# Performance work log

Hardware: AMD Instinct MI355X
Metric: run time of the kernel (lower is better)

The kernel has to match this reference:

```python
import jax, jax.numpy as jnp
import numpy as np

EPS = 1e-5

def ter_quant(w):
    # BitNet b1.58 absmean ternary quantization: scale by mean(|W|), round to {-1,0,1}, rescale.
    gamma = jnp.mean(jnp.abs(w)) + EPS
    wq = jnp.clip(jnp.round(w / gamma), -1.0, 1.0) * gamma
    return wq

def setup_inputs() -> dict:
    key = jax.random.key(0)
    k_x, k_w1, k_w2 = jax.random.split(key, 3)
    B, S, D, H = 64, 197, 768, 3072
    x = jax.random.normal(k_x, (B, S, D), dtype=jnp.float32)
    w1 = jax.random.normal(k_w1, (H, D), dtype=jnp.float32) * (1.0 / np.sqrt(D))
    b1 = jnp.zeros((H,), dtype=jnp.float32)
    w2 = jax.random.normal(k_w2, (D, H), dtype=jnp.float32) * (1.0 / np.sqrt(H))
    b2 = jnp.zeros((D,), dtype=jnp.float32)
    return {"x": x, "w1": w1, "b1": b1, "w2": w2, "b2": b2}

def reference(x, w1, b1, w2, b2):
    # fc1: ternary-quantized linear, exact GELU, fc2: ternary-quantized linear (dropout p=0 is identity)
    h = jnp.einsum('bsd,hd->bsh', x, ter_quant(w1)) + b1
    h = jax.nn.gelu(h, approximate=False)
    y = jnp.einsum('bsh,dh->bsd', h, ter_quant(w2)) + b2
    return y
```

## Files before the change

kernel.cpp:

```cpp
#include <hip/hip_runtime.h>
#include <hip/hip_bf16.h>
#include <math.h>

typedef __bf16 bf16_t;
typedef __bf16 bf16x8 __attribute__((ext_vector_type(8)));
typedef __bf16 bf16x4 __attribute__((ext_vector_type(4)));
typedef float f32x4 __attribute__((ext_vector_type(4)));

#define QEPS 1e-5

__device__ __forceinline__ void gload_lds16(const void* g, void* l) {
  __builtin_amdgcn_global_load_lds((const __attribute__((address_space(1))) void*)g,
                                   (__attribute__((address_space(3))) void*)l, 16, 0, 0);
}

__device__ __forceinline__ float gelu_exact(float x) {
  float a = x * 0.7071067811865476f;
  float s = fabsf(a);
  float t = __builtin_amdgcn_rcpf(__builtin_fmaf(0.3275911f, s, 1.0f));
  float p = __builtin_fmaf(1.061405429f, t, -1.453152027f);
  p = __builtin_fmaf(p, t, 1.421413741f);
  p = __builtin_fmaf(p, t, -0.284496736f);
  p = __builtin_fmaf(p, t, 0.254829592f);
  p = p * t;
  float e = __expf(-s * s);
  float er = copysignf(__builtin_fmaf(-p, e, 1.0f), a);
  return 0.5f * x * (1.0f + er);
}

__global__ void reduce_part_kernel(const float* __restrict__ w1, const float* __restrict__ w2,
                                   int n, double* __restrict__ part) {
  const bool second = blockIdx.x >= 256;
  const float* __restrict__ w = second ? w2 : w1;
  const int b = second ? blockIdx.x - 256 : blockIdx.x;
  double s = 0.0;
  const int stride = 256 * 256 * 4;
  for (int i = (b * 256 + threadIdx.x) * 4; i < n; i += stride) {
    float4 v = *(const float4*)(w + i);
    s += (double)fabsf(v.x) + (double)fabsf(v.y) + (double)fabsf(v.z) + (double)fabsf(v.w);
  }
  for (int off = 32; off > 0; off >>= 1)
    s += __shfl_down(s, off, 64);
  __shared__ double ls[4];
  int lane = threadIdx.x & 63, wv = threadIdx.x >> 6;
  if (lane == 0) ls[wv] = s;
  __syncthreads();
  if (threadIdx.x == 0) part[blockIdx.x] = ls[0] + ls[1] + ls[2] + ls[3];
}

__global__ void prep_kernel(const float* __restrict__ w1, const float* __restrict__ w2,
                            const float* __restrict__ x, const double* __restrict__ part,
                            int nW, long long nxv, bf16_t* __restrict__ q1,
                            bf16_t* __restrict__ q2, bf16_t* __restrict__ xb,
                            double* __restrict__ gammas) {
  const int QB = (nW >> 1) >> 8;
  const int tid = threadIdx.x;
  if (blockIdx.x < QB) {
    const int half = QB >> 1;
    const bool second = blockIdx.x >= half;
    double p = part[(second ? 256 : 0) + tid];
    for (int off = 32; off > 0; off >>= 1)
      p += __shfl_down(p, off, 64);
    __shared__ double red[4];
    if ((tid & 63) == 0) red[tid >> 6] = p;
    __syncthreads();
    const double g = (red[0] + red[1] + red[2] + red[3]) / (double)nW + QEPS;
    if (tid == 0 && blockIdx.x == (second ? half : 0)) gammas[second ? 1 : 0] = g;
    const double rg = 1.0 / g;
    const int idx = blockIdx.x * 256 + tid - (second ? (nW >> 2) : 0);
    const float4 v = ((const float4*)(second ? w2 : w1))[idx];
    bf16x4 r;
    r[0] = (bf16_t)(float)fmin(1.0, fmax(-1.0, rint((double)v.x * rg)));
    r[1] = (bf16_t)(float)fmin(1.0, fmax(-1.0, rint((double)v.y * rg)));
    r[2] = (bf16_t)(float)fmin(1.0, fmax(-1.0, rint((double)v.z * rg)));
    r[3] = (bf16_t)(float)fmin(1.0, fmax(-1.0, rint((double)v.w * rg)));
    ((bf16x4*)(second ? q2 : q1))[idx] = r;
  } else {
    long long i = ((long long)(blockIdx.x - QB) * 256 + tid) * 4;
    bf16x4 r;
    if (i < nxv) {
      float4 v = *(const float4*)(x + i);
      r[0] = (bf16_t)v.x; r[1] = (bf16_t)v.y; r[2] = (bf16_t)v.z; r[3] = (bf16_t)v.w;
    } else {
      r[0] = (bf16_t)0.0f; r[1] = (bf16_t)0.0f; r[2] = (bf16_t)0.0f; r[3] = (bf16_t)0.0f;
    }
    *(bf16x4*)(xb + i) = r;
  }
}

template <int EPI, int BN>
__global__ __launch_bounds__(256, 4)
void gemm_bt_kernel(const bf16_t* __restrict__ A, const bf16_t* __restrict__ B,
                    const float* __restrict__ bias, const double* __restrict__ gptr,
                    void* __restrict__ Cout, int N, int K, int Mvalid, int gx) {
  constexpr int NJ = BN / 32;
  __shared__ bf16_t sA[128 * 64];
  __shared__ bf16_t sB[BN * 64];

  const int G = gridDim.x;
  const int f = blockIdx.x;
  const int xcd = f & 7;
  const int idx = f >> 3;
  const int q8 = G >> 3, r8 = G & 7;
  const int t = xcd * q8 + (xcd < r8 ? xcd : r8) + idx;
  const int bx = t % gx;
  const int by = t / gx;

  const int tid = threadIdx.x;
  const int lane = tid & 63;
  const int wave = tid >> 6;
  const int wr = (wave >> 1) * 64;
  const int wc = (wave & 1) * (BN / 2);
  const int row16 = lane & 15;
  const int quad = lane >> 4;

  const size_t Ks = (size_t)K;
  const int cg = (tid & 7) ^ ((tid >> 3) & 7);
  const bf16_t* gA = A + ((size_t)(by * 128 + (tid >> 3))) * Ks + (size_t)cg * 8;
  const bf16_t* gB = B + ((size_t)(bx * BN + (tid >> 3))) * Ks + (size_t)cg * 8;
  bf16_t* lA = sA + wave * 512;
  bf16_t* lB = sB + wave * 512;

  f32x4 acc[4][NJ] = {};

  for (int k0 = 0; k0 < K; k0 += 64) {
#pragma unroll
    for (int n = 0; n < 4; n++)
      gload_lds16(gA + (size_t)(n * 32) * Ks, lA + n * 2048);
#pragma unroll
    for (int n = 0; n < BN / 32; n++)
      gload_lds16(gB + (size_t)(n * 32) * Ks, lB + n * 2048);
    gA += 64;
    gB += 64;
    __syncthreads();

#pragma unroll
    for (int kk = 0; kk < 2; kk++) {
      bf16x8 afr[4], bfr[NJ];
      const int swz = ((kk * 4 + quad) ^ (row16 & 7)) * 8;
#pragma unroll
      for (int i = 0; i < 4; i++)
        afr[i] = *(const bf16x8*)&sA[(wr + i * 16 + row16) * 64 + swz];
#pragma unroll
      for (int j = 0; j < NJ; j++)
        bfr[j] = *(const bf16x8*)&sB[(wc + j * 16 + row16) * 64 + swz];
#pragma unroll
      for (int i = 0; i < 4; i++)
#pragma unroll
        for (int j = 0; j < NJ; j++)
          acc[i][j] = __builtin_amdgcn_mfma_f32_16x16x32_bf16(afr[i], bfr[j], acc[i][j], 0, 0, 0);
    }
    __syncthreads();
  }

  const float gamma = (float)gptr[0];
  const int c_base = bx * BN + wc + row16;
  const int r_base = by * 128 + wr + quad * 4;

  if constexpr (EPI == 0) {
    bf16_t* sE = sA;
    float bv[NJ];
#pragma unroll
    for (int j = 0; j < NJ; j++) bv[j] = bias[c_base + j * 16];
    bf16_t* h = (bf16_t*)Cout;
#pragma unroll
    for (int i = 0; i < 4; i++) {
#pragma unroll
      for (int j = 0; j < NJ; j++) {
        const int col = wc + j * 16 + row16;
#pragma unroll
        for (int r = 0; r < 4; r++) {
          const int e = (wave >> 1) * 16 + quad * 4 + r;
          float v = gelu_exact(gamma * acc[i][j][r] + bv[j]);
          sE[e * 136 + col] = (bf16_t)v;
        }
      }
      __syncthreads();
      {
        const int e = tid >> 3, ch = tid & 7;
        const int grow = by * 128 + (e >> 4) * 64 + i * 16 + (e & 15);
        bf16_t* dst = &h[(size_t)grow * N + bx * BN];
        *(bf16x8*)&dst[ch * 8] = *(const bf16x8*)&sE[e * 136 + ch * 8];
        *(bf16x8*)&dst[ch * 8 + 64] = *(const bf16x8*)&sE[e * 136 + ch * 8 + 64];
      }
      __syncthreads();
    }
  } else {
    float* out = (float*)Cout;
#pragma unroll
    for (int j = 0; j < NJ; j++) {
      const int col = c_base + j * 16;
      const float bv = bias[col];
#pragma unroll
      for (int i = 0; i < 4; i++) {
#pragma unroll
        for (int r = 0; r < 4; r++) {
          const int row = r_base + i * 16 + r;
          if (row < Mvalid)
            out[(size_t)row * N + col] = gamma * acc[i][j][r] + bv;
        }
      }
    }
  }
}

extern "C" void kernel_launch(void* const* d_in, const int* in_sizes, int n_in,
                              void* d_out, int out_size, void* d_ws, size_t ws_size,
                              hipStream_t stream) {
  const float* x  = (const float*)d_in[0];
  const float* w1 = (const float*)d_in[1];
  const float* b1 = (const float*)d_in[2];
  const float* w2 = (const float*)d_in[3];
  const float* b2 = (const float*)d_in[4];
  float* out = (float*)d_out;

  const int M = 64 * 197;
  const int Mpad = 12672;
  const int D = 768, H = 3072;
  const int nW = H * D;

  char* ws = (char*)d_ws;
  double* part = (double*)ws;
  double* gammas = (double*)(ws + 4096);
  bf16_t* xb  = (bf16_t*)(ws + 4096 + 256);
  bf16_t* w1q = xb + (size_t)Mpad * D;
  bf16_t* w2q = w1q + (size_t)H * D;
  bf16_t* hb  = w2q + (size_t)D * H;

  reduce_part_kernel<<<512, 256, 0, stream>>>(w1, w2, nW, part);
  const int QB = (nW >> 1) >> 8;
  const int CB = (int)(((long long)Mpad * D / 4) / 256);
  prep_kernel<<<QB + CB, 256, 0, stream>>>(w1, w2, x, part, nW, (long long)M * D,
                                           w1q, w2q, xb, gammas);

  const int gy = Mpad / 128;
  const int gx1 = H / 128;
  const int gx2 = D / 64;
  gemm_bt_kernel<0, 128><<<gx1 * gy, 256, 0, stream>>>(xb, w1q, b1, gammas + 0, hb, H, D, M, gx1);
  gemm_bt_kernel<1, 64><<<gx2 * gy, 256, 0, stream>>>(hb, w2q, b2, gammas + 1, out, D, H, M, gx2);
}
```

Before: 258.4 us.

## Double-buffer LDS tiles in GEMM and use 128x128 tiles for both GEMMs

Adds two LDS stages so the global-to-LDS loads for the next K slice are issued before computing on the current slice, which overlaps memory latency with MFMA work and removes one barrier per iteration. The second GEMM moves from 128x64 to 128x128 tiles, giving more reuse of each loaded tile. LDS use grows to 64KB per block and launch bounds drop to 2 blocks per CU, which reduces occupancy. The fc2 grid also becomes smaller (6 column tiles), which may leave the machine less evenly loaded.

```diff
diff --git a/kernel.cpp b/kernel.cpp
--- a/kernel.cpp
+++ b/kernel.cpp
@@ -88,14 +88,12 @@
   }
 }
 
-template <int EPI, int BN>
-__global__ __launch_bounds__(256, 4)
+template <int EPI>
+__global__ __launch_bounds__(256, 2)
 void gemm_bt_kernel(const bf16_t* __restrict__ A, const bf16_t* __restrict__ B,
                     const float* __restrict__ bias, const double* __restrict__ gptr,
                     void* __restrict__ Cout, int N, int K, int Mvalid, int gx) {
-  constexpr int NJ = BN / 32;
-  __shared__ bf16_t sA[128 * 64];
-  __shared__ bf16_t sB[BN * 64];
+  __shared__ bf16_t sm[2][2][128 * 64];
 
   const int G = gridDim.x;
   const int f = blockIdx.x;
@@ -110,63 +108,75 @@
   const int lane = tid & 63;
   const int wave = tid >> 6;
   const int wr = (wave >> 1) * 64;
-  const int wc = (wave & 1) * (BN / 2);
+  const int wc = (wave & 1) * 64;
   const int row16 = lane & 15;
   const int quad = lane >> 4;
 
   const size_t Ks = (size_t)K;
   const int cg = (tid & 7) ^ ((tid >> 3) & 7);
   const bf16_t* gA = A + ((size_t)(by * 128 + (tid >> 3))) * Ks + (size_t)cg * 8;
-  const bf16_t* gB = B + ((size_t)(bx * BN + (tid >> 3))) * Ks + (size_t)cg * 8;
-  bf16_t* lA = sA + wave * 512;
-  bf16_t* lB = sB + wave * 512;
-
-  f32x4 acc[4][NJ] = {};
-
+  const bf16_t* gB = B + ((size_t)(bx * 128 + (tid >> 3))) * Ks + (size_t)cg * 8;
+  const int lofs = wave * 512;
+
+  f32x4 acc[4][4] = {};
+
+#pragma unroll
+  for (int n = 0; n < 4; n++) {
+    gload_lds16(gA + (size_t)(n * 32) * Ks, &sm[0][0][lofs + n * 2048]);
+    gload_lds16(gB + (size_t)(n * 32) * Ks, &sm[0][1][lofs + n * 2048]);
+  }
+  gA += 64;
+  gB += 64;
+  __syncthreads();
+
+  int p = 0;
   for (int k0 = 0; k0 < K; k0 += 64) {
-#pragma unroll
-    for (int n = 0; n < 4; n++)
-      gload_lds16(gA + (size_t)(n * 32) * Ks, lA + n * 2048);
-#pragma unroll
-    for (int n = 0; n < BN / 32; n++)
-      gload_lds16(gB + (size_t)(n * 32) * Ks, lB + n * 2048);
-    gA += 64;
-    gB += 64;
-    __syncthreads();
-
+    if (k0 + 64 < K) {
+#pragma unroll
+      for (int n = 0; n < 4; n++) {
+        gload_lds16(gA + (size_t)(n * 32) * Ks, &sm[p ^ 1][0][lofs + n * 2048]);
+        gload_lds16(gB + (size_t)(n * 32) * Ks, &sm[p ^ 1][1][lofs + n * 2048]);
+      }
+      gA += 64;
+      gB += 64;
+    }
+
+    const bf16_t* sA = sm[p][0];
+    const bf16_t* sB = sm[p][1];
 #pragma unroll
     for (int kk = 0; kk < 2; kk++) {
-      bf16x8 afr[4], bfr[NJ];
+      bf16x8 afr[4], bfr[4];
       const int swz = ((kk * 4 + quad) ^ (row16 & 7)) * 8;
 #pragma unroll
       for (int i = 0; i < 4; i++)
         afr[i] = *(const bf16x8*)&sA[(wr + i * 16 + row16) * 64 + swz];
 #pragma unroll
-      for (int j = 0; j < NJ; j++)
+      for (int j = 0; j < 4; j++)
         bfr[j] = *(const bf16x8*)&sB[(wc + j * 16 + row16) * 64 + swz];
 #pragma unroll
       for (int i = 0; i < 4; i++)
 #pragma unroll
-        for (int j = 0; j < NJ; j++)
+        for (int j = 0; j < 4; j++)
           acc[i][j] = __builtin_amdgcn_mfma_f32_16x16x32_bf16(afr[i], bfr[j], acc[i][j], 0, 0, 0);
     }
     __syncthreads();
+    p ^= 1;
   }
 
   const float gamma = (float)gptr[0];
-  const int c_base = bx * BN + wc + row16;
+  const int c_base = bx * 128 + wc + row16;
   const int r_base = by * 128 + wr + quad * 4;
 
   if constexpr (EPI == 0) {
-    bf16_t* sE = sA;
-    float bv[NJ];
-#pragma unroll
-    for (int j = 0; j < NJ; j++) bv[j] = bias[c_base + j * 16];
+    bf16_t* sE = &sm[0][0][0];
+    float bv[4];
+#pragma unroll
+    for (int j = 0; j < 4; j++) bv[j] = bias[c_base + j * 16];
     bf16_t* h = (bf16_t*)Cout;
 #pragma unroll
     for (int i = 0; i < 4; i++) {
 #pragma unroll
-      for (int j = 0; j < NJ; j++) {
+      for (int j = 0; j < 4; j++) {
         const int col = wc + j * 16 + row16;
 #pragma unroll
         for (int r = 0; r < 4; r++) {
@@ -179,7 +189,7 @@
       {
         const int e = tid >> 3, ch = tid & 7;
         const int grow = by * 128 + (e >> 4) * 64 + i * 16 + (e & 15);
-        bf16_t* dst = &h[(size_t)grow * N + bx * BN];
+        bf16_t* dst = &h[(size_t)grow * N + bx * 128];
         *(bf16x8*)&dst[ch * 8] = *(const bf16x8*)&sE[e * 136 + ch * 8];
         *(bf16x8*)&dst[ch * 8 + 64] = *(const bf16x8*)&sE[e * 136 + ch * 8 + 64];
       }
@@ -188,7 +198,7 @@
   } else {
     float* out = (float*)Cout;
 #pragma unroll
-    for (int j = 0; j < NJ; j++) {
+    for (int j = 0; j < 4; j++) {
       const int col = c_base + j * 16;
       const float bv = bias[col];
 #pragma unroll
@@ -235,7 +245,7 @@
 
   const int gy = Mpad / 128;
   const int gx1 = H / 128;
-  const int gx2 = D / 64;
-  gemm_bt_kernel<0, 128><<<gx1 * gy, 256, 0, stream>>>(xb, w1q, b1, gammas + 0, hb, H, D, M, gx1);
-  gemm_bt_kernel<1, 64><<<gx2 * gy, 256, 0, stream>>>(hb, w2q, b2, gammas + 1, out, D, H, M, gx2);
-}
+  const int gx2 = D / 128;
+  gemm_bt_kernel<0><<<gx1 * gy, 256, 0, stream>>>(xb, w1q, b1, gammas + 0, hb, H, D, M, gx1);
+  gemm_bt_kernel<1><<<gx2 * gy, 256, 0, stream>>>(hb, w2q, b2, gammas + 1, out, D, H, M, gx2);
+}
```

New measurement: 279.6 us. 8.2% more time.

## Pre-tile operands into swizzled K-chunks and double-buffer LDS in GEMMs

Applied to the files above, without the earlier changes.

The prep kernel now writes x, w1q and w2q into a blocked layout of 128x32 tiles with an XOR swizzle. GEMM1's epilogue writes h in the same blocked layout, so each GEMM loads contiguous 8KB tiles and LDS is double-buffered over K=32 steps, with one barrier per step. GEMM1 tile width grows to 256 columns, giving fewer blocks with more accumulators each. This is meant to overlap global loads with MFMA work and get fully coalesced loads, at the cost of more LDS per block, lower occupancy and hardcoded problem sizes.

```diff
diff --git a/kernel.cpp b/kernel.cpp
--- a/kernel.cpp
+++ b/kernel.cpp
@@ -4,7 +4,6 @@
 
 typedef __bf16 bf16_t;
 typedef __bf16 bf16x8 __attribute__((ext_vector_type(8)));
-typedef __bf16 bf16x4 __attribute__((ext_vector_type(4)));
 typedef float f32x4 __attribute__((ext_vector_type(4)));
 
 #define QEPS 1e-5
@@ -50,52 +49,70 @@
 
 __global__ void prep_kernel(const float* __restrict__ w1, const float* __restrict__ w2,
                             const float* __restrict__ x, const double* __restrict__ part,
-                            int nW, long long nxv, bf16_t* __restrict__ q1,
-                            bf16_t* __restrict__ q2, bf16_t* __restrict__ xb,
-                            double* __restrict__ gammas) {
-  const int QB = (nW >> 1) >> 8;
+                            double* __restrict__ gammas, bf16_t* __restrict__ q1,
+                            bf16_t* __restrict__ q2, bf16_t* __restrict__ xb) {
   const int tid = threadIdx.x;
-  if (blockIdx.x < QB) {
-    const int half = QB >> 1;
-    const bool second = blockIdx.x >= half;
+  const int b = blockIdx.x;
+  if (b < 2304) {
+    const bool second = b >= 1152;
     double p = part[(second ? 256 : 0) + tid];
     for (int off = 32; off > 0; off >>= 1)
       p += __shfl_down(p, off, 64);
     __shared__ double red[4];
     if ((tid & 63) == 0) red[tid >> 6] = p;
     __syncthreads();
-    const double g = (red[0] + red[1] + red[2] + red[3]) / (double)nW + QEPS;
-    if (tid == 0 && blockIdx.x == (second ? half : 0)) gammas[second ? 1 : 0] = g;
+    const double g = (red[0] + red[1] + red[2] + red[3]) / 2359296.0 + QEPS;
+    if (tid == 0 && (b == 0 || b == 1152)) gammas[second ? 1 : 0] = g;
     const double rg = 1.0 / g;
-    const int idx = blockIdx.x * 256 + tid - (second ? (nW >> 2) : 0);
-    const float4 v = ((const float4*)(second ? w2 : w1))[idx];
-    bf16x4 r;
-    r[0] = (bf16_t)(float)fmin(1.0, fmax(-1.0, rint((double)v.x * rg)));
-    r[1] = (bf16_t)(float)fmin(1.0, fmax(-1.0, rint((double)v.y * rg)));
-    r[2] = (bf16_t)(float)fmin(1.0, fmax(-1.0, rint((double)v.z * rg)));
-    r[3] = (bf16_t)(float)fmin(1.0, fmax(-1.0, rint((double)v.w * rg)));
-    ((bf16x4*)(second ? q2 : q1))[idx] = r;
+    const int gchunk = (second ? b - 1152 : b) * 256 + tid;
+    const int tile = gchunk >> 9, cidx = gchunk & 511;
+    const int r = cidx >> 2, slot = cidx & 3, cch = slot ^ (r & 3);
+    int row, colbase, C;
+    if (second) { C = 3072; row = (tile / 96) * 128 + r; colbase = (tile % 96) * 32 + cch * 8; }
+    else        { C = 768;  row = (tile / 24) * 128 + r; colbase = (tile % 24) * 32 + cch * 8; }
+    const float* __restrict__ W = second ? w2 : w1;
+    const float4 v0 = *(const float4*)(W + (size_t)row * C + colbase);
+    const float4 v1 = *(const float4*)(W + (size_t)row * C + colbase + 4);
+    bf16x8 o;
+    o[0] = (bf16_t)(float)fmin(1.0, fmax(-1.0, rint((double)v0.x * rg)));
+    o[1] = (bf16_t)(float)fmin(1.0, fmax(-1.0, rint((double)v0.y * rg)));
+    o[2] = (bf16_t)(float)fmin(1.0, fmax(-1.0, rint((double)v0.z * rg)));
+    o[3] = (bf16_t)(float)fmin(1.0, fmax(-1.0, rint((double)v0.w * rg)));
+    o[4] = (bf16_t)(float)fmin(1.0, fmax(-1.0, rint((double)v1.x * rg)));
+    o[5] = (bf16_t)(float)fmin(1.0, fmax(-1.0, rint((double)v1.y * rg)));
+    o[6] = (bf16_t)(float)fmin(1.0, fmax(-1.0, rint((double)v1.z * rg)));
+    o[7] = (bf16_t)(float)fmin(1.0, fmax(-1.0, rint((double)v1.w * rg)));
+    *(bf16x8*)((second ? q2 : q1) + (size_t)gchunk * 8) = o;
   } else {
-    long long i = ((long long)(blockIdx.x - QB) * 256 + tid) * 4;
-    bf16x4 r;
-    if (i < nxv) {
-      float4 v = *(const float4*)(x + i);
-      r[0] = (bf16_t)v.x; r[1] = (bf16_t)v.y; r[2] = (bf16_t)v.z; r[3] = (bf16_t)v.w;
+    const int gchunk = (b - 2304) * 256 + tid;
+    const int tile = gchunk >> 9, cidx = gchunk & 511;
+    const int r = cidx >> 2, slot = cidx & 3, cch = slot ^ (r & 3);
+    const int row = (tile / 24) * 128 + r;
+    const int colbase = (tile % 24) * 32 + cch * 8;
+    bf16x8 o;
+    if (row < 12608) {
+      const float4 v0 = *(const float4*)(x + (size_t)row * 768 + colbase);
+      const float4 v1 = *(const float4*)(x + (size_t)row * 768 + colbase + 4);
+      o[0] = (bf16_t)v0.x; o[1] = (bf16_t)v0.y; o[2] = (bf16_t)v0.z; o[3] = (bf16_t)v0.w;
+      o[4] = (bf16_t)v1.x; o[5] = (bf16_t)v1.y; o[6] = (bf16_t)v1.z; o[7] = (bf16_t)v1.w;
     } else {
-      r[0] = (bf16_t)0.0f; r[1] = (bf16_t)0.0f; r[2] = (bf16_t)0.0f; r[3] = (bf16_t)0.0f;
-    }
-    *(bf16x4*)(xb + i) = r;
-  }
-}
-
-template <int EPI, int BN>
-__global__ __launch_bounds__(256, 4)
-void gemm_bt_kernel(const bf16_t* __restrict__ A, const bf16_t* __restrict__ B,
-                    const float* __restrict__ bias, const double* __restrict__ gptr,
-                    void* __restrict__ Cout, int N, int K, int Mvalid, int gx) {
-  constexpr int NJ = BN / 32;
-  __shared__ bf16_t sA[128 * 64];
-  __shared__ bf16_t sB[BN * 64];
+      o = bf16x8{};
+    }
+    *(bf16x8*)(xb + (size_t)gchunk * 8) = o;
+  }
+}
+
+template <int EPI, int NJ>
+__global__ __launch_bounds__(256, (NJ == 8 ? 2 : 3))
+void gemm_tiled(const bf16_t* __restrict__ A, const bf16_t* __restrict__ B,
+                const float* __restrict__ bias, const double* __restrict__ gptr,
+                void* __restrict__ Cout, int nkt, int gx, int Mvalid, int aux) {
+  constexpr int BN = NJ * 32;
+  constexpr int BTILE = BN * 32;
+  constexpr int NRTB = BN / 128;
+  __shared__ bf16_t sm[2 * 4096 + 2 * BTILE];
+  bf16_t* const sA0 = sm;
+  bf16_t* const sB0 = sm + 2 * 4096;
 
   const int G = gridDim.x;
   const int f = blockIdx.x;
@@ -114,55 +131,72 @@
   const int row16 = lane & 15;
   const int quad = lane >> 4;
 
-  const size_t Ks = (size_t)K;
-  const int cg = (tid & 7) ^ ((tid >> 3) & 7);
-  const bf16_t* gA = A + ((size_t)(by * 128 + (tid >> 3))) * Ks + (size_t)cg * 8;
-  const bf16_t* gB = B + ((size_t)(bx * BN + (tid >> 3))) * Ks + (size_t)cg * 8;
-  bf16_t* lA = sA + wave * 512;
-  bf16_t* lB = sB + wave * 512;
+  const bf16_t* gA = A + ((size_t)by * nkt) * 4096 + tid * 8;
+  const bf16_t* gB0 = B + ((size_t)(bx * NRTB) * nkt) * 4096 + tid * 8;
+  const bf16_t* gB1 = (NJ == 8) ? B + ((size_t)(bx * NRTB + 1) * nkt) * 4096 + tid * 8 : nullptr;
+  const int lws = wave * 512;
 
   f32x4 acc[4][NJ] = {};
 
-  for (int k0 = 0; k0 < K; k0 += 64) {
-#pragma unroll
-    for (int n = 0; n < 4; n++)
-      gload_lds16(gA + (size_t)(n * 32) * Ks, lA + n * 2048);
-#pragma unroll
-    for (int n = 0; n < BN / 32; n++)
-      gload_lds16(gB + (size_t)(n * 32) * Ks, lB + n * 2048);
-    gA += 64;
-    gB += 64;
+  {
+    gload_lds16(gA, sA0 + lws);
+    gload_lds16(gA + 2048, sA0 + 2048 + lws);
+    gload_lds16(gB0, sB0 + lws);
+    gload_lds16(gB0 + 2048, sB0 + 2048 + lws);
+    if constexpr (NJ == 8) {
+      gload_lds16(gB1, sB0 + 4096 + lws);
+      gload_lds16(gB1 + 2048, sB0 + 6144 + lws);
+    }
+    gA += 4096; gB0 += 4096;
+    if constexpr (NJ == 8) gB1 += 4096;
+  }
+  __syncthreads();
+
+  int p = 0;
+  const int sw = (quad ^ (row16 & 3)) * 8;
+  for (int kt = 0; kt < nkt; kt++) {
+    if (kt + 1 < nkt) {
+      bf16_t* dA = sA0 + (p ^ 1) * 4096;
+      bf16_t* dB = sB0 + (p ^ 1) * BTILE;
+      gload_lds16(gA, dA + lws);
+      gload_lds16(gA + 2048, dA + 2048 + lws);
+      gload_lds16(gB0, dB + lws);
+      gload_lds16(gB0 + 2048, dB + 2048 + lws);
+      if constexpr (NJ == 8) {
+        gload_lds16(gB1, dB + 4096 + lws);
+        gload_lds16(gB1 + 2048, dB + 6144 + lws);
+      }
+      gA += 4096; gB0 += 4096;
+      if constexpr (NJ == 8) gB1 += 4096;
+    }
+    const bf16_t* sA = sA0 + p * 4096;
+    const bf16_t* sB = sB0 + p * BTILE;
+    bf16x8 afr[4], bfr[NJ];
+#pragma unroll
+    for (int i = 0; i < 4; i++)
+      afr[i] = *(const bf16x8*)&sA[(wr + i * 16 + row16) * 32 + sw];
+#pragma unroll
+    for (int j = 0; j < NJ; j++)
+      bfr[j] = *(const bf16x8*)&sB[(wc + j * 16 + row16) * 32 + sw];
+#pragma unroll
+    for (int i = 0; i < 4; i++)
+#pragma unroll
+      for (int j = 0; j < NJ; j++)
+        acc[i][j] = __builtin_amdgcn_mfma_f32_16x16x32_bf16(afr[i], bfr[j], acc[i][j], 0, 0, 0);
     __syncthreads();
-
-#pragma unroll
-    for (int kk = 0; kk < 2; kk++) {
-      bf16x8 afr[4], bfr[NJ];
-      const int swz = ((kk * 4 + quad) ^ (row16 & 7)) * 8;
-#pragma unroll
-      for (int i = 0; i < 4; i++)
-        afr[i] = *(const bf16x8*)&sA[(wr + i * 16 + row16) * 64 + swz];
-#pragma unroll
-      for (int j = 0; j < NJ; j++)
-        bfr[j] = *(const bf16x8*)&sB[(wc + j * 16 + row16) * 64 + swz];
-#pragma unroll
-      for (int i = 0; i < 4; i++)
-#pragma unroll
-        for (int j = 0; j < NJ; j++)
-          acc[i][j] = __builtin_amdgcn_mfma_f32_16x16x32_bf16(afr[i], bfr[j], acc[i][j], 0, 0, 0);
-    }
-    __syncthreads();
+    p ^= 1;
   }
 
   const float gamma = (float)gptr[0];
-  const int c_base = bx * BN + wc + row16;
-  const int r_base = by * 128 + wr + quad * 4;
 
   if constexpr (EPI == 0) {
-    bf16_t* sE = sA;
+    constexpr int SEW = BN + 8;
+    bf16_t* sE = sm;
+    bf16_t* h = (bf16_t*)Cout;
     float bv[NJ];
 #pragma unroll
-    for (int j = 0; j < NJ; j++) bv[j] = bias[c_base + j * 16];
-    bf16_t* h = (bf16_t*)Cout;
+    for (int j = 0; j < NJ; j++) bv[j] = bias[bx * BN + wc + row16 + j * 16];
+    const int ktBase = bx * (BN / 32);
 #pragma unroll
     for (int i = 0; i < 4; i++) {
 #pragma unroll
@@ -171,22 +205,28 @@
 #pragma unroll
         for (int r = 0; r < 4; r++) {
           const int e = (wave >> 1) * 16 + quad * 4 + r;
-          float v = gelu_exact(gamma * acc[i][j][r] + bv[j]);
-          sE[e * 136 + col] = (bf16_t)v;
+          sE[e * SEW + col] = (bf16_t)gelu_exact(gamma * acc[i][j][r] + bv[j]);
         }
       }
       __syncthreads();
       {
-        const int e = tid >> 3, ch = tid & 7;
-        const int grow = by * 128 + (e >> 4) * 64 + i * 16 + (e & 15);
-        bf16_t* dst = &h[(size_t)grow * N + bx * BN];
-        *(bf16x8*)&dst[ch * 8] = *(const bf16x8*)&sE[e * 136 + ch * 8];
-        *(bf16x8*)&dst[ch * 8 + 64] = *(const bf16x8*)&sE[e * 136 + ch * 8 + 64];
+        const int e2 = tid >> 3, chb = tid & 7;
+        const int r_in = (e2 >> 4) * 64 + i * 16 + (e2 & 15);
+#pragma unroll
+        for (int cc = 0; cc < BN / 64; cc++) {
+          const int c = chb + cc * 8;
+          const int kt_o = ktBase + (c >> 2);
+          const int slot = (c & 3) ^ (r_in & 3);
+          const size_t off = ((size_t)(by * aux + kt_o)) * 4096 + r_in * 32 + slot * 8;
+          *(bf16x8*)&h[off] = *(const bf16x8*)&sE[e2 * SEW + c * 8];
+        }
       }
       __syncthreads();
     }
   } else {
     float* out = (float*)Cout;
+    const int c_base = bx * BN + wc + row16;
+    const int r_base = by * 128 + wr + quad * 4;
 #pragma unroll
     for (int j = 0; j < NJ; j++) {
       const int col = c_base + j * 16;
@@ -197,7 +237,7 @@
         for (int r = 0; r < 4; r++) {
           const int row = r_base + i * 16 + r;
           if (row < Mvalid)
-            out[(size_t)row * N + col] = gamma * acc[i][j][r] + bv;
+            out[(size_t)row * aux + col] = gamma * acc[i][j][r] + bv;
         }
       }
     }
@@ -228,14 +268,8 @@
   bf16_t* hb  = w2q + (size_t)D * H;
 
   reduce_part_kernel<<<512, 256, 0, stream>>>(w1, w2, nW, part);
-  const int QB = (nW >> 1) >> 8;
-  const int CB = (int)(((long long)Mpad * D / 4) / 256);
-  prep_kernel<<<QB + CB, 256, 0, stream>>>(w1, w2, x, part, nW, (long long)M * D,
-                                           w1q, w2q, xb, gammas);
-
-  const int gy = Mpad / 128;
-  const int gx1 = H / 128;
-  const int gx2 = D / 64;
-  gemm_bt_kernel<0, 128><<<gx1 * gy, 256, 0, stream>>>(xb, w1q, b1, gammas + 0, hb, H, D, M, gx1);
-  gemm_bt_kernel<1, 64><<<gx2 * gy, 256, 0, stream>>>(hb, w2q, b2, gammas + 1, out, D, H, M, gx2);
-}
+  prep_kernel<<<2304 + 4752, 256, 0, stream>>>(w1, w2, x, part, gammas, w1q, w2q, xb);
+
+  gemm_tiled<0, 8><<<99 * 12, 256, 0, stream>>>(xb, w1q, b1, gammas + 0, hb, 24, 12, M, H / 32);
+  gemm_tiled<1, 4><<<99 * 6, 256, 0, stream>>>(hb, w2q, b2, gammas + 1, out, 96, 6, M, D);
+}
```

Result: faster. 252.5 us (-2.3%).
